# Performance work log

Measured on AMD Instinct MI355X. Metric: run time of the kernel, lower is better.

Reference implementation:

```python
import jax, jax.numpy as jnp
import numpy as np

H, W, C = 96, 96, 21
THETA_ALPHA, THETA_BETA, THETA_GAMMA = 8.0, 0.125, 3.0
NUM_ITERATIONS = 5


def setup_inputs() -> dict:
    key = jax.random.key(0)
    k1, k2, k3, k4, k5 = jax.random.split(key, 5)
    unaries = jax.random.normal(k1, (1, H, W, C), dtype=jnp.float32)
    reference_image = jax.random.uniform(k2, (1, H, W, 3), dtype=jnp.float32)
    # truncated normal(mean=0, std=0.1) as in tf.initializers.truncated_normal
    spatial_ker_weights = 0.1 * jax.random.truncated_normal(k3, -2.0, 2.0, (C,), dtype=jnp.float32)
    bilateral_ker_weights = 0.1 * jax.random.truncated_normal(k4, -2.0, 2.0, (C,), dtype=jnp.float32)
    compatibility_matrix = 0.1 * jax.random.truncated_normal(k5, -2.0, 2.0, (C, C), dtype=jnp.float32)
    return {
        "unaries": unaries,
        "reference_image": reference_image,
        "spatial_ker_weights": spatial_ker_weights,
        "bilateral_ker_weights": bilateral_ker_weights,
        "compatibility_matrix": compatibility_matrix,
    }


def _gaussian_kernel(feats):
    # feats: [B, N, D] -> K[b, i, j] = exp(-0.5 * ||f_i - f_j||^2)
    sq = jnp.sum(feats * feats, axis=-1)  # [B, N]
    d2 = sq[:, :, None] + sq[:, None, :] - 2.0 * jnp.einsum("bnd,bmd->bnm", feats, feats)
    return jnp.exp(-0.5 * jnp.maximum(d2, 0.0))


def _build_kernels(reference_image):
    # Exact-math equivalent of the permutohedral lattice Gaussian filter:
    # spatial features = positions/theta_gamma; bilateral = [pos/theta_alpha, rgb/theta_beta].
    B = reference_image.shape[0]
    yy, xx = jnp.meshgrid(jnp.arange(H, dtype=jnp.float32), jnp.arange(W, dtype=jnp.float32), indexing="ij")
    pos = jnp.stack([yy, xx], axis=-1).reshape(1, H * W, 2)  # [1, N, 2]
    pos = jnp.broadcast_to(pos, (B, H * W, 2))
    col = reference_image.reshape(B, H * W, 3)
    k_spatial = _gaussian_kernel(pos / THETA_GAMMA)
    k_bilateral = _gaussian_kernel(jnp.concatenate([pos / THETA_ALPHA, col / THETA_BETA], axis=-1))
    return k_spatial, k_bilateral


def reference(unaries, reference_image, spatial_ker_weights, bilateral_ker_weights, compatibility_matrix):
    B = unaries.shape[0]
    N = H * W
    k_spatial, k_bilateral = _build_kernels(reference_image)  # built once; reused each iteration
    u = unaries.reshape(B, N, C)
    q = u
    for _ in range(NUM_ITERATIONS):
        q = jax.nn.softmax(q, axis=-1)
        spatial_out = jnp.einsum("bnm,bmc->bnc", k_spatial, q)
        bilateral_out = jnp.einsum("bnm,bmc->bnc", k_bilateral, q)
        # pairwise^T = compat @ diag(w_s) @ S^T + compat @ diag(w_b) @ Bi^T
        # => pairwise = (S * w_s + Bi * w_b) @ compat^T
        message = spatial_out * spatial_ker_weights + bilateral_out * bilateral_ker_weights
        pairwise = message @ compatibility_matrix.T
        q = u - pairwise
    return q.reshape(unaries.shape)
```

## Files before the change

kernel.cpp:

```cpp
#include <hip/hip_runtime.h>
#include <hip/hip_bf16.h>
#include <algorithm>
#include <cmath>

#define HH 96
#define WW 96
#define CC 21
#define NN (HH*WW)
#define NELEM (NN*CC)
#define RS 20
#define NPAR (2*CC + CC*CC)
#define L2E 1.4426950408889634f
#define MSTEPS 24
#define NBB (36*24)
#define NSTRIP 8
#define NBLUR (CC*NSTRIP)
#define SROWS 12
#define TRUNC2 1225
#define BLURKEY 0x10000

typedef short bf16x8 __attribute__((ext_vector_type(8)));
typedef float f32x16 __attribute__((ext_vector_type(16)));

__device__ __forceinline__ float fexp2(float x) { return __builtin_amdgcn_exp2f(x); }
__device__ __forceinline__ float fexp(float x)  { return __builtin_amdgcn_exp2f(x * L2E); }

__device__ __forceinline__ short f2b(float f) {
    __hip_bfloat16 h = __float2bfloat16(f);
    short s; __builtin_memcpy(&s, &h, 2); return s;
}

__global__ void k_sniff(const unsigned short* __restrict__ u16, int* __restrict__ flag32) {
    __shared__ int sfound;
    if (threadIdx.x == 0) sfound = 0;
    __syncthreads();
    const int base = blockIdx.x * (NELEM/32);
    int found = 0;
    for (int i = base + threadIdx.x; i < base + NELEM/32; i += 256) {
        unsigned v = u16[i];
        if ((v & 0x7F80u) == 0x7F80u) found = 1;
    }
    if (found) sfound = 1;
    __syncthreads();
    if (threadIdx.x == 0) flag32[blockIdx.x] = sfound;
}

__device__ __forceinline__ int rdflag(const int* __restrict__ flag32) {
    int f = 0;
    #pragma unroll
    for (int i = 0; i < 32; i++) f |= flag32[i];
    return f;
}

__global__ __launch_bounds__(256) void k_prep(
    const void* __restrict__ u, const void* __restrict__ img,
    const void* __restrict__ wS, const void* __restrict__ wB,
    const void* __restrict__ compat, const int* __restrict__ flag32,
    float* __restrict__ uf, float* __restrict__ featx, float* __restrict__ par,
    float* __restrict__ bil, __hip_bfloat16* __restrict__ pT)
{
    const int f = rdflag(flag32);
    const int tid = threadIdx.x;
    const int n = blockIdx.x * 256 + tid;

    if (blockIdx.x == 0) {
        for (int i = tid; i < NPAR; i += 256) {
            const void* src; int j;
            if (i < CC)        { src = wS;     j = i; }
            else if (i < 2*CC) { src = wB;     j = i - CC; }
            else               { src = compat; j = i - 2*CC; }
            par[i] = f ? ((const float*)src)[j]
                       : __bfloat162float(((const __hip_bfloat16*)src)[j]);
        }
    }

    {
        float c0, c1, c2;
        if (f) { const float* p = (const float*)img;
                 c0 = p[3*n]; c1 = p[3*n+1]; c2 = p[3*n+2]; }
        else   { const __hip_bfloat16* p = (const __hip_bfloat16*)img;
                 c0 = __bfloat162float(p[3*n]); c1 = __bfloat162float(p[3*n+1]);
                 c2 = __bfloat162float(p[3*n+2]); }
        float ym = (float)(n / WW), xm = (float)(n % WW);
        const float sc = 0.15014029f;
        const float cf = 9.6089787f;
        featx[8*n + 0] = -L2E * (fmaf(ym, ym, xm*xm) * 0.0078125f
                                 + 32.f * (c0*c0 + c1*c1 + c2*c2));
        featx[8*n + 1] = sc * ym;
        featx[8*n + 2] = sc * xm;
        featx[8*n + 3] = cf * c0;
        featx[8*n + 4] = cf * c1;
        featx[8*n + 5] = cf * c2;
        featx[8*n + 6] = 0.f;
        featx[8*n + 7] = 0.f;
    }

    float v[CC];
    float mx = -1e30f;
    #pragma unroll
    for (int c = 0; c < CC; c++) {
        float uv = f ? ((const float*)u)[n*CC + c]
                     : __bfloat162float(((const __hip_bfloat16*)u)[n*CC + c]);
        uf[n*CC + c] = uv;
        v[c] = uv;
        mx = fmaxf(mx, uv);
    }
    float s = 0.f;
    #pragma unroll
    for (int c = 0; c < CC; c++) { v[c] = fexp(v[c] - mx); s += v[c]; }
    float inv = 1.f / s;
    #pragma unroll
    for (int c = 0; c < CC; c++) {
        pT[(size_t)c*NN + n] = __float2bfloat16(v[c] * inv);
        bil[(size_t)c*NN + n] = 0.f;
    }
}

__global__ __launch_bounds__(256) void k_work(
    const __hip_bfloat16* __restrict__ pT,
    const float* __restrict__ featx,
    float* __restrict__ bil,
    float* __restrict__ s2T,
    const int* __restrict__ tab)
{
    __shared__ float smem[6176];
    const int tid = threadIdx.x;
    const int item = tab[blockIdx.x];

    if (item < BLURKEY) {
        float* lds_h = smem;
        const int wv   = tid >> 6, lane = tid & 63;
        const int quad = lane >> 5, lid = lane & 31;

        const int nt = item >> 5, mc = item & 31;
        const int ny0 = (nt / 6) * 16, nx0 = (nt % 6) * 16;
        const int my0 = (mc & 3) * 24, mx0 = (mc >> 2) * 16;

        const int dx = (mx0 > nx0 + 15) ? mx0 - (nx0 + 15)
                     : ((nx0 > mx0 + 15) ? nx0 - (mx0 + 15) : 0);
        const int lim = TRUNC2 - dx * dx;
        int T = (int)sqrtf((float)lim);
        T -= (T * T > lim);
        T += ((T + 1) * (T + 1) <= lim);

        int blo = ny0 - T - my0;      blo = blo < 0 ? 0 : blo;
        int bhi = ny0 + 15 + T - my0; bhi = bhi > 23 ? 23 : bhi;

        {
            float4* dst = (float4*)lds_h;
            for (int i = blo * 32 + tid; i < (bhi + 1) * 32; i += 256) {
                const int seg = i >> 5, off = i & 31;
                dst[i] = ((const float4*)(featx +
                          (size_t)((my0 + seg) * WW + mx0) * 8))[off];
            }
        }
        __syncthreads();

        const int by0 = ny0 + 4 * wv;
        int lo = by0 - T - my0;     lo = lo < 0 ? 0 : lo;
        int hi = by0 + 3 + T - my0; hi = hi > 23 ? 23 : hi;
        if (lo > hi) return;

        const int row = lid >> 4, col = lid & 15;
        const int n0 = (by0 + row) * WW + nx0 + col;
        const int n1 = n0 + 2 * WW;
        const float4 g0a = *(const float4*)(featx + (size_t)n0 * 8);
        const float4 g0b = *(const float4*)(featx + (size_t)n0 * 8 + 4);
        const float4 g1a = *(const float4*)(featx + (size_t)n1 * 8);
        const float4 g1b = *(const float4*)(featx + (size_t)n1 * 8 + 4);

        f32x16 acc0, acc1;
        #pragma unroll
        for (int r = 0; r < 16; r++) { acc0[r] = 0.f; acc1[r] = 0.f; }

        int mg = (my0 + lo) * WW + mx0 + quad * 8;
        #pragma unroll 1
        for (int step = lo; step <= hi; step++, mg += WW) {
            bf16x8 afrag = *(const bf16x8*)(pT + (size_t)lid * NN + mg);

            const float* h = lds_h + (step * 16 + quad * 8) * 8;
            float kb0[8], kb1[8];
            #pragma unroll
            for (int j = 0; j < 8; j++) {
                float4 ha = *(const float4*)(h + j * 8);
                float4 hb = *(const float4*)(h + j * 8 + 4);
                float s0 = g0a.x + ha.x;
                s0 = fmaf(g0a.y, ha.y, s0);
                s0 = fmaf(g0a.z, ha.z, s0);
                s0 = fmaf(g0a.w, ha.w, s0);
                s0 = fmaf(g0b.x, hb.x, s0);
                s0 = fmaf(g0b.y, hb.y, s0);
                kb0[j] = fexp2(s0);
                float s1 = g1a.x + ha.x;
                s1 = fmaf(g1a.y, ha.y, s1);
                s1 = fmaf(g1a.z, ha.z, s1);
                s1 = fmaf(g1a.w, ha.w, s1);
                s1 = fmaf(g1b.x, hb.x, s1);
                s1 = fmaf(g1b.y, hb.y, s1);
                kb1[j] = fexp2(s1);
            }
            bf16x8 b0, b1;
            #pragma unroll
            for (int j = 0; j < 8; j++) { b0[j] = f2b(kb0[j]); b1[j] = f2b(kb1[j]); }

            acc0 = __builtin_amdgcn_mfma_f32_32x32x16_bf16(afrag, b0, acc0, 0, 0, 0);
            acc1 = __builtin_amdgcn_mfma_f32_32x32x16_bf16(afrag, b1, acc1, 0, 0, 0);
        }

        #pragma unroll
        for (int r = 0; r < 16; r++) {
            int c = (r & 3) + 8 * (r >> 2) + 4 * quad;
            if (c < CC) {
                atomicAdd(&bil[(size_t)c * NN + n0], acc0[r]);
                atomicAdd(&bil[(size_t)c * NN + n1], acc1[r]);
            }
        }
    } else {
        __shared__ float w_s[RS + 1];
        float* A  = smem;
        float* B2 = smem + 4992;

        const int b2 = item - BLURKEY;
        const int c = b2 % CC;
        const int strip = b2 / CC;
        const int y0 = strip * SROWS;
        const int ylo = (y0 - RS < 0) ? 0 : y0 - RS;
        const int yhi = (y0 + SROWS - 1 + RS > HH - 1) ? HH - 1 : y0 + SROWS - 1 + RS;
        const int nrows = yhi - ylo + 1;

        if (tid <= RS) w_s[tid] = fexp2(-(float)(tid*tid) * (L2E / 18.f));
        const __hip_bfloat16* src = pT + (size_t)c * NN + ylo * WW;
        for (int i = tid; i < nrows * WW; i += 256)
            A[i] = __bfloat162float(src[i]);
        __syncthreads();

        for (int i = tid; i < SROWS * WW; i += 256) {
            const int yo = y0 + i / WW;
            const int x  = i % WW;
            float acc = A[(yo - ylo) * WW + x];
            #pragma unroll
            for (int d = 1; d <= RS; d++) {
                float s = 0.f;
                if (yo - d >= 0)  s += A[(yo - d - ylo) * WW + x];
                if (yo + d < HH)  s += A[(yo + d - ylo) * WW + x];
                acc = fmaf(w_s[d], s, acc);
            }
            B2[i] = acc;
        }
        __syncthreads();

        for (int i = tid; i < SROWS * WW; i += 256) {
            const int r = i / WW, x = i % WW;
            float acc = B2[i];
            #pragma unroll
            for (int d = 1; d <= RS; d++) {
                float s = 0.f;
                if (x - d >= 0)  s += B2[r * WW + x - d];
                if (x + d < WW)  s += B2[r * WW + x + d];
                acc = fmaf(w_s[d], s, acc);
            }
            s2T[(size_t)c * NN + (y0 + r) * WW + x] = acc;
        }
    }
}

__global__ __launch_bounds__(256) void k_update(
    float* __restrict__ bil, const float* __restrict__ s2T,
    const float* __restrict__ uf, const float* __restrict__ par,
    const int* __restrict__ flag32,
    __hip_bfloat16* __restrict__ pT, void* __restrict__ out, int last)
{
    __shared__ float sc[CC*CC + 1];
    __shared__ float sws[CC], swb[CC];
    const int tid = threadIdx.x;
    for (int i = tid; i < CC*CC; i += 256) sc[i] = par[2*CC + i];
    if (tid == 0) sc[CC*CC] = 0.f;
    if (tid < CC) { sws[tid] = par[tid]; swb[tid] = par[CC + tid]; }
    __syncthreads();

    const int half = tid & 1;
    const int n = blockIdx.x * 128 + (tid >> 1);

    float msg[11];
    #pragma unroll
    for (int k = 0; k < 11; k++) {
        const int cp = 2*k + half;
        if (cp < CC) {
            msg[k] = fmaf(s2T[(size_t)cp*NN + n], sws[cp],
                          bil[(size_t)cp*NN + n] * swb[cp]);
            bil[(size_t)cp*NN + n] = 0.f;
        } else msg[k] = 0.f;
    }

    float pw[CC];
    #pragma unroll
    for (int c = 0; c < CC; c++) {
        float a = msg[0] * sc[c*CC + half];
        #pragma unroll
        for (int k = 1; k < 11; k++)
            a = fmaf(msg[k], sc[c*CC + 2*k + half], a);
        pw[c] = a;
    }
    #pragma unroll
    for (int c = 0; c < CC; c++)
        pw[c] += __shfl_xor(pw[c], 1, 64);

    float qv[CC];
    float mx = -1e30f;
    #pragma unroll
    for (int c = 0; c < CC; c++) {
        qv[c] = uf[(size_t)n*CC + c] - pw[c];
        mx = fmaxf(mx, qv[c]);
    }

    if (last) {
        const int is_f32 = rdflag(flag32);
        #pragma unroll
        for (int k = 0; k < 11; k++) {
            const int ce = 2*k, co = (k < 10) ? 2*k + 1 : 0;
            float v = half ? qv[co] : qv[ce];
            const int c = 2*k + half;
            if (c < CC) {
                if (is_f32) ((float*)out)[(size_t)n*CC + c] = v;
                else ((__hip_bfloat16*)out)[(size_t)n*CC + c] = __float2bfloat16(v);
            }
        }
    } else {
        float ex[11]; float ssum = 0.f;
        #pragma unroll
        for (int k = 0; k < 11; k++) {
            const int ce = 2*k, co = (k < 10) ? 2*k + 1 : 0;
            float v = half ? qv[co] : qv[ce];
            float e = fexp(v - mx);
            if (2*k + half < CC) ssum += e;
            ex[k] = e;
        }
        ssum += __shfl_xor(ssum, 1, 64);
        const float inv = 1.f / ssum;
        #pragma unroll
        for (int k = 0; k < 11; k++) {
            const int c = 2*k + half;
            if (c < CC) pT[(size_t)c*NN + n] = __float2bfloat16(ex[k] * inv);
        }
    }
}

extern "C" void kernel_launch(void* const* d_in, const int* in_sizes, int n_in,
                              void* d_out, int out_size, void* d_ws, size_t ws_size,
                              hipStream_t stream)
{
    static int h_tab[NBB + NBLUR];
    static int h_n = 0;
    if (h_n == 0) {
        struct It { int key; int cost; };
        static It its[NBB + NBLUR];
        int m = 0;
        for (int nt = 0; nt < 36; nt++)
            for (int mc = 0; mc < 24; mc++) {
                const int ny0 = (nt / 6) * 16, nx0 = (nt % 6) * 16;
                const int my0 = (mc & 3) * 24, mx0 = (mc >> 2) * 16;
                const int dx = (mx0 > nx0 + 15) ? mx0 - (nx0 + 15)
                             : ((nx0 > mx0 + 15) ? nx0 - (mx0 + 15) : 0);
                const int lim = TRUNC2 - dx * dx;
                if (lim < 0) continue;
                int T = (int)std::sqrt((double)lim);
                while (T * T > lim) T--;
                while ((T + 1) * (T + 1) <= lim) T++;
                int cost = 0;
                for (int wv = 0; wv < 4; wv++) {
                    const int by0 = ny0 + 4 * wv;
                    int lo = by0 - T - my0;     if (lo < 0)  lo = 0;
                    int hi = by0 + 3 + T - my0; if (hi > 23) hi = 23;
                    if (lo <= hi) cost += hi - lo + 1;
                }
                if (cost == 0) continue;
                its[m].key = (nt << 5) | mc; its[m].cost = cost; m++;
            }
        for (int b = 0; b < NBLUR; b++) { its[m].key = BLURKEY + b; its[m].cost = 20; m++; }
        std::sort(its, its + m, [](const It& a, const It& b) { return a.cost > b.cost; });
        for (int i = 0; i < m; i++) h_tab[i] = its[i].key;
        h_n = m;
    }

    float* ws = (float*)d_ws;
    int*   flag32 = (int*)ws;
    float* par    = ws + 32;
    float* featx  = ws + 544;
    __hip_bfloat16* pT = (__hip_bfloat16*)(ws + 74272);
    float* uf  = ws + 74272 + 147456;
    float* s2T = uf + NELEM;
    float* bil = s2T + NELEM;
    int*   d_tab = (int*)(bil + NELEM);

    hipMemcpyAsync(d_tab, h_tab, h_n * sizeof(int), hipMemcpyHostToDevice, stream);

    k_sniff<<<32, 256, 0, stream>>>((const unsigned short*)d_in[0], flag32);
    k_prep<<<NN/256, 256, 0, stream>>>(d_in[0], d_in[1], d_in[2], d_in[3], d_in[4],
                                       flag32, uf, featx, par, bil, pT);

    for (int it = 0; it < 5; it++) {
        k_work<<<h_n, 256, 0, stream>>>(pT, featx, bil, s2T, d_tab);
        k_update<<<NN/128, 256, 0, stream>>>(bil, s2T, uf, par, flag32,
                                             pT, d_out, (it == 4) ? 1 : 0);
    }
}
```

Measured before the change: 237.9 us.

## Bin bilateral m-chunks per tile into register-accumulated slots instead of atomics

Work items for the bilateral product are regrouped on the host so that each output tile gets up to eight load-balanced bins of m-chunks. Each block loops over its chunks, accumulating in MFMA registers, then writes plain stores to a per-slot buffer instead of issuing float atomicAdds. The update kernel sums the eight slots and zeroes them. This removes atomic contention and per-block setup overhead. In exchange, each iteration reads and clears eight full-size slot buffers, and each block does more serial work and sync per chunk.

```diff
diff --git a/kernel.cpp b/kernel.cpp
--- a/kernel.cpp
+++ b/kernel.cpp
@@ -1,6 +1,7 @@
 #include <hip/hip_runtime.h>
 #include <hip/hip_bf16.h>
 #include <algorithm>
+#include <vector>
 #include <cmath>
 
 #define HH 96
@@ -11,13 +12,11 @@
 #define RS 20
 #define NPAR (2*CC + CC*CC)
 #define L2E 1.4426950408889634f
-#define MSTEPS 24
-#define NBB (36*24)
-#define NSTRIP 8
-#define NBLUR (CC*NSTRIP)
+#define NSLOT 8
 #define SROWS 12
+#define NBLUR (CC*8)
 #define TRUNC2 1225
-#define BLURKEY 0x10000
+#define BLURFLAG 0x40000000
 
 typedef short bf16x8 __attribute__((ext_vector_type(8)));
 typedef float f32x16 __attribute__((ext_vector_type(16)));
@@ -57,7 +56,7 @@
     const void* __restrict__ wS, const void* __restrict__ wB,
     const void* __restrict__ compat, const int* __restrict__ flag32,
     float* __restrict__ uf, float* __restrict__ featx, float* __restrict__ par,
-    float* __restrict__ bil, __hip_bfloat16* __restrict__ pT)
+    float* __restrict__ bil8, __hip_bfloat16* __restrict__ pT)
 {
     const int f = rdflag(flag32);
     const int tid = threadIdx.x;
@@ -73,7 +72,6 @@
                        : __bfloat162float(((const __hip_bfloat16*)src)[j]);
         }
     }
-
     {
         float c0, c1, c2;
         if (f) { const float* p = (const float*)img;
@@ -112,56 +110,80 @@
     #pragma unroll
     for (int c = 0; c < CC; c++) {
         pT[(size_t)c*NN + n] = __float2bfloat16(v[c] * inv);
-        bil[(size_t)c*NN + n] = 0.f;
+        #pragma unroll
+        for (int sl = 0; sl < NSLOT; sl++)
+            bil8[((size_t)sl*CC + c)*NN + n] = 0.f;
+    }
+}
+
+__device__ __forceinline__ void blur_item(
+    int b2, float* smem, const __hip_bfloat16* __restrict__ pT,
+    float* __restrict__ s2T, int tid)
+{
+    float* A   = smem;
+    float* B2  = smem + 4992;
+    float* w_s = smem + 6144;
+    const int c = b2 % CC;
+    const int strip = b2 / CC;
+    const int y0 = strip * SROWS;
+    const int ylo = (y0 - RS < 0) ? 0 : y0 - RS;
+    const int yhi = (y0 + SROWS - 1 + RS > HH - 1) ? HH - 1 : y0 + SROWS - 1 + RS;
+    const int nrows = yhi - ylo + 1;
+
+    if (tid <= RS) w_s[tid] = fexp2(-(float)(tid*tid) * (L2E / 18.f));
+    const __hip_bfloat16* src = pT + (size_t)c * NN + ylo * WW;
+    for (int i = tid; i < nrows * WW; i += 256)
+        A[i] = __bfloat162float(src[i]);
+    __syncthreads();
+
+    for (int i = tid; i < SROWS * WW; i += 256) {
+        const int yo = y0 + i / WW;
+        const int x  = i % WW;
+        float acc = A[(yo - ylo) * WW + x];
+        #pragma unroll
+        for (int d = 1; d <= RS; d++) {
+            float s = 0.f;
+            if (yo - d >= 0)  s += A[(yo - d - ylo) * WW + x];
+            if (yo + d < HH)  s += A[(yo + d - ylo) * WW + x];
+            acc = fmaf(w_s[d], s, acc);
+        }
+        B2[i] = acc;
+    }
+    __syncthreads();
+
+    for (int i = tid; i < SROWS * WW; i += 256) {
+        const int r = i / WW, x = i % WW;
+        float acc = B2[i];
+        #pragma unroll
+        for (int d = 1; d <= RS; d++) {
+            float s = 0.f;
+            if (x - d >= 0)  s += B2[r * WW + x - d];
+            if (x + d < WW)  s += B2[r * WW + x + d];
+            acc = fmaf(w_s[d], s, acc);
+        }
+        s2T[(size_t)c * NN + (y0 + r) * WW + x] = acc;
     }
 }
 
 __global__ __launch_bounds__(256) void k_work(
-    const __hip_bfloat16* __restrict__ pT,
-    const float* __restrict__ featx,
-    float* __restrict__ bil,
-    float* __restrict__ s2T,
-    const int* __restrict__ tab)
+    const __hip_bfloat16* __restrict__ pT, const float* __restrict__ featx,
+    float* __restrict__ bil8, float* __restrict__ s2T,
+    const int* __restrict__ hdr, const int* __restrict__ mcs)
 {
     __shared__ float smem[6176];
     const int tid = threadIdx.x;
-    const int item = tab[blockIdx.x];
-
-    if (item < BLURKEY) {
-        float* lds_h = smem;
-        const int wv   = tid >> 6, lane = tid & 63;
+    const int item = hdr[blockIdx.x];
+
+    if (!(item & BLURFLAG)) {
+        const int nt   = item >> 18;
+        const int slot = (item >> 15) & 7;
+        const int off  = (item >> 5) & 1023;
+        const int cnt  = item & 31;
+        const int ny0 = (nt / 6) * 16, nx0 = (nt % 6) * 16;
+        const int wv = tid >> 6, lane = tid & 63;
         const int quad = lane >> 5, lid = lane & 31;
-
-        const int nt = item >> 5, mc = item & 31;
-        const int ny0 = (nt / 6) * 16, nx0 = (nt % 6) * 16;
-        const int my0 = (mc & 3) * 24, mx0 = (mc >> 2) * 16;
-
-        const int dx = (mx0 > nx0 + 15) ? mx0 - (nx0 + 15)
-                     : ((nx0 > mx0 + 15) ? nx0 - (mx0 + 15) : 0);
-        const int lim = TRUNC2 - dx * dx;
-        int T = (int)sqrtf((float)lim);
-        T -= (T * T > lim);
-        T += ((T + 1) * (T + 1) <= lim);
-
-        int blo = ny0 - T - my0;      blo = blo < 0 ? 0 : blo;
-        int bhi = ny0 + 15 + T - my0; bhi = bhi > 23 ? 23 : bhi;
-
-        {
-            float4* dst = (float4*)lds_h;
-            for (int i = blo * 32 + tid; i < (bhi + 1) * 32; i += 256) {
-                const int seg = i >> 5, off = i & 31;
-                dst[i] = ((const float4*)(featx +
-                          (size_t)((my0 + seg) * WW + mx0) * 8))[off];
-            }
-        }
-        __syncthreads();
-
+        const int row = lid >> 4, col = lid & 15;
         const int by0 = ny0 + 4 * wv;
-        int lo = by0 - T - my0;     lo = lo < 0 ? 0 : lo;
-        int hi = by0 + 3 + T - my0; hi = hi > 23 ? 23 : hi;
-        if (lo > hi) return;
-
-        const int row = lid >> 4, col = lid & 15;
         const int n0 = (by0 + row) * WW + nx0 + col;
         const int n1 = n0 + 2 * WW;
         const float4 g0a = *(const float4*)(featx + (size_t)n0 * 8);
@@ -173,99 +195,77 @@
         #pragma unroll
         for (int r = 0; r < 16; r++) { acc0[r] = 0.f; acc1[r] = 0.f; }
 
-        int mg = (my0 + lo) * WW + mx0 + quad * 8;
-        #pragma unroll 1
-        for (int step = lo; step <= hi; step++, mg += WW) {
-            bf16x8 afrag = *(const bf16x8*)(pT + (size_t)lid * NN + mg);
-
-            const float* h = lds_h + (step * 16 + quad * 8) * 8;
-            float kb0[8], kb1[8];
-            #pragma unroll
-            for (int j = 0; j < 8; j++) {
-                float4 ha = *(const float4*)(h + j * 8);
-                float4 hb = *(const float4*)(h + j * 8 + 4);
-                float s0 = g0a.x + ha.x;
-                s0 = fmaf(g0a.y, ha.y, s0);
-                s0 = fmaf(g0a.z, ha.z, s0);
-                s0 = fmaf(g0a.w, ha.w, s0);
-                s0 = fmaf(g0b.x, hb.x, s0);
-                s0 = fmaf(g0b.y, hb.y, s0);
-                kb0[j] = fexp2(s0);
-                float s1 = g1a.x + ha.x;
-                s1 = fmaf(g1a.y, ha.y, s1);
-                s1 = fmaf(g1a.z, ha.z, s1);
-                s1 = fmaf(g1a.w, ha.w, s1);
-                s1 = fmaf(g1b.x, hb.x, s1);
-                s1 = fmaf(g1b.y, hb.y, s1);
-                kb1[j] = fexp2(s1);
-            }
-            bf16x8 b0, b1;
-            #pragma unroll
-            for (int j = 0; j < 8; j++) { b0[j] = f2b(kb0[j]); b1[j] = f2b(kb1[j]); }
-
-            acc0 = __builtin_amdgcn_mfma_f32_32x32x16_bf16(afrag, b0, acc0, 0, 0, 0);
-            acc1 = __builtin_amdgcn_mfma_f32_32x32x16_bf16(afrag, b1, acc1, 0, 0, 0);
+        for (int ci = 0; ci < cnt; ci++) {
+            const int mc = mcs[off + ci];
+            const int my0 = (mc & 3) * 24, mx0 = (mc >> 2) * 16;
+            const int dx = (mx0 > nx0 + 15) ? mx0 - (nx0 + 15)
+                         : ((nx0 > mx0 + 15) ? nx0 - (mx0 + 15) : 0);
+            const int lim = TRUNC2 - dx * dx;
+            int T = (int)sqrtf((float)lim);
+            T -= (T * T > lim);
+            T += ((T + 1) * (T + 1) <= lim);
+            int blo = ny0 - T - my0;      blo = blo < 0 ? 0 : blo;
+            int bhi = ny0 + 15 + T - my0; bhi = bhi > 23 ? 23 : bhi;
+
+            __syncthreads();
+            {
+                float4* dst = (float4*)smem;
+                for (int i = blo * 32 + tid; i < (bhi + 1) * 32; i += 256) {
+                    const int seg = i >> 5, o = i & 31;
+                    dst[i] = ((const float4*)(featx +
+                              (size_t)((my0 + seg) * WW + mx0) * 8))[o];
+                }
+            }
+            __syncthreads();
+
+            int lo = by0 - T - my0;     lo = lo < 0 ? 0 : lo;
+            int hi = by0 + 3 + T - my0; hi = hi > 23 ? 23 : hi;
+            if (lo <= hi) {
+                int mg = (my0 + lo) * WW + mx0 + quad * 8;
+                #pragma unroll 1
+                for (int step = lo; step <= hi; step++, mg += WW) {
+                    bf16x8 afrag = *(const bf16x8*)(pT + (size_t)lid * NN + mg);
+                    const float* h = smem + (step * 16 + quad * 8) * 8;
+                    float kb0[8], kb1[8];
+                    #pragma unroll
+                    for (int j = 0; j < 8; j++) {
+                        float4 ha = *(const float4*)(h + j * 8);
+                        float4 hb = *(const float4*)(h + j * 8 + 4);
+                        float s0 = g0a.x + ha.x;
+                        s0 = fmaf(g0a.y, ha.y, s0); s0 = fmaf(g0a.z, ha.z, s0);
+                        s0 = fmaf(g0a.w, ha.w, s0); s0 = fmaf(g0b.x, hb.x, s0);
+                        s0 = fmaf(g0b.y, hb.y, s0);
+                        kb0[j] = fexp2(s0);
+                        float s1 = g1a.x + ha.x;
+                        s1 = fmaf(g1a.y, ha.y, s1); s1 = fmaf(g1a.z, ha.z, s1);
+                        s1 = fmaf(g1a.w, ha.w, s1); s1 = fmaf(g1b.x, hb.x, s1);
+                        s1 = fmaf(g1b.y, hb.y, s1);
+                        kb1[j] = fexp2(s1);
+                    }
+                    bf16x8 b0, b1;
+                    #pragma unroll
+                    for (int j = 0; j < 8; j++) { b0[j] = f2b(kb0[j]); b1[j] = f2b(kb1[j]); }
+                    acc0 = __builtin_amdgcn_mfma_f32_32x32x16_bf16(afrag, b0, acc0, 0, 0, 0);
+                    acc1 = __builtin_amdgcn_mfma_f32_32x32x16_bf16(afrag, b1, acc1, 0, 0, 0);
+                }
+            }
         }
 
         #pragma unroll
         for (int r = 0; r < 16; r++) {
             int c = (r & 3) + 8 * (r >> 2) + 4 * quad;
             if (c < CC) {
-                atomicAdd(&bil[(size_t)c * NN + n0], acc0[r]);
-                atomicAdd(&bil[(size_t)c * NN + n1], acc1[r]);
+                bil8[((size_t)slot*CC + c)*NN + n0] = acc0[r];
+                bil8[((size_t)slot*CC + c)*NN + n1] = acc1[r];
             }
         }
     } else {
-        __shared__ float w_s[RS + 1];
-        float* A  = smem;
-        float* B2 = smem + 4992;
-
-        const int b2 = item - BLURKEY;
-        const int c = b2 % CC;
-        const int strip = b2 / CC;
-        const int y0 = strip * SROWS;
-        const int ylo = (y0 - RS < 0) ? 0 : y0 - RS;
-        const int yhi = (y0 + SROWS - 1 + RS > HH - 1) ? HH - 1 : y0 + SROWS - 1 + RS;
-        const int nrows = yhi - ylo + 1;
-
-        if (tid <= RS) w_s[tid] = fexp2(-(float)(tid*tid) * (L2E / 18.f));
-        const __hip_bfloat16* src = pT + (size_t)c * NN + ylo * WW;
-        for (int i = tid; i < nrows * WW; i += 256)
-            A[i] = __bfloat162float(src[i]);
-        __syncthreads();
-
-        for (int i = tid; i < SROWS * WW; i += 256) {
-            const int yo = y0 + i / WW;
-            const int x  = i % WW;
-            float acc = A[(yo - ylo) * WW + x];
-            #pragma unroll
-            for (int d = 1; d <= RS; d++) {
-                float s = 0.f;
-                if (yo - d >= 0)  s += A[(yo - d - ylo) * WW + x];
-                if (yo + d < HH)  s += A[(yo + d - ylo) * WW + x];
-                acc = fmaf(w_s[d], s, acc);
-            }
-            B2[i] = acc;
-        }
-        __syncthreads();
-
-        for (int i = tid; i < SROWS * WW; i += 256) {
-            const int r = i / WW, x = i % WW;
-            float acc = B2[i];
-            #pragma unroll
-            for (int d = 1; d <= RS; d++) {
-                float s = 0.f;
-                if (x - d >= 0)  s += B2[r * WW + x - d];
-                if (x + d < WW)  s += B2[r * WW + x + d];
-                acc = fmaf(w_s[d], s, acc);
-            }
-            s2T[(size_t)c * NN + (y0 + r) * WW + x] = acc;
-        }
+        blur_item(item & 0xFFFF, smem, pT, s2T, tid);
     }
 }
 
 __global__ __launch_bounds__(256) void k_update(
-    float* __restrict__ bil, const float* __restrict__ s2T,
+    float* __restrict__ bil8, const float* __restrict__ s2T,
     const float* __restrict__ uf, const float* __restrict__ par,
     const int* __restrict__ flag32,
     __hip_bfloat16* __restrict__ pT, void* __restrict__ out, int last)
@@ -286,9 +286,14 @@
     for (int k = 0; k < 11; k++) {
         const int cp = 2*k + half;
         if (cp < CC) {
-            msg[k] = fmaf(s2T[(size_t)cp*NN + n], sws[cp],
-                          bil[(size_t)cp*NN + n] * swb[cp]);
-            bil[(size_t)cp*NN + n] = 0.f;
+            float b = 0.f;
+            #pragma unroll
+            for (int sl = 0; sl < NSLOT; sl++)
+                b += bil8[((size_t)sl*CC + cp)*NN + n];
+            msg[k] = fmaf(s2T[(size_t)cp*NN + n], sws[cp], b * swb[cp]);
+            #pragma unroll
+            for (int sl = 0; sl < NSLOT; sl++)
+                bil8[((size_t)sl*CC + cp)*NN + n] = 0.f;
         } else msg[k] = 0.f;
     }
 
@@ -349,37 +354,64 @@
                               void* d_out, int out_size, void* d_ws, size_t ws_size,
                               hipStream_t stream)
 {
-    static int h_tab[NBB + NBLUR];
-    static int h_n = 0;
-    if (h_n == 0) {
-        struct It { int key; int cost; };
-        static It its[NBB + NBLUR];
-        int m = 0;
-        for (int nt = 0; nt < 36; nt++)
+    static std::vector<int> h_buf;
+    static int h_nb = 0;
+    if (h_nb == 0) {
+        struct Rec { int blur, b2, nt, slot; long load; std::vector<int> mc; };
+        std::vector<Rec> recs;
+        for (int nt = 0; nt < 36; nt++) {
+            const int ny0 = (nt/6)*16, nx0 = (nt%6)*16;
+            struct It { int mc; int cost; };
+            std::vector<It> v; long tot = 0;
             for (int mc = 0; mc < 24; mc++) {
-                const int ny0 = (nt / 6) * 16, nx0 = (nt % 6) * 16;
-                const int my0 = (mc & 3) * 24, mx0 = (mc >> 2) * 16;
-                const int dx = (mx0 > nx0 + 15) ? mx0 - (nx0 + 15)
-                             : ((nx0 > mx0 + 15) ? nx0 - (mx0 + 15) : 0);
-                const int lim = TRUNC2 - dx * dx;
+                const int my0 = (mc&3)*24, mx0 = (mc>>2)*16;
+                const int dx = (mx0 > nx0+15) ? mx0-(nx0+15)
+                             : ((nx0 > mx0+15) ? nx0-(mx0+15) : 0);
+                const int lim = TRUNC2 - dx*dx;
                 if (lim < 0) continue;
                 int T = (int)std::sqrt((double)lim);
-                while (T * T > lim) T--;
-                while ((T + 1) * (T + 1) <= lim) T++;
+                while (T*T > lim) T--;
+                while ((T+1)*(T+1) <= lim) T++;
                 int cost = 0;
                 for (int wv = 0; wv < 4; wv++) {
-                    const int by0 = ny0 + 4 * wv;
+                    const int by0 = ny0 + 4*wv;
                     int lo = by0 - T - my0;     if (lo < 0)  lo = 0;
                     int hi = by0 + 3 + T - my0; if (hi > 23) hi = 23;
                     if (lo <= hi) cost += hi - lo + 1;
                 }
                 if (cost == 0) continue;
-                its[m].key = (nt << 5) | mc; its[m].cost = cost; m++;
-            }
-        for (int b = 0; b < NBLUR; b++) { its[m].key = BLURKEY + b; its[m].cost = 20; m++; }
-        std::sort(its, its + m, [](const It& a, const It& b) { return a.cost > b.cost; });
-        for (int i = 0; i < m; i++) h_tab[i] = its[i].key;
-        h_n = m;
+                v.push_back({mc, cost}); tot += cost;
+            }
+            if (v.empty()) continue;
+            int nb = (int)std::min<long>(NSLOT, (tot + 159) / 160);
+            if (nb > (int)v.size()) nb = (int)v.size();
+            std::sort(v.begin(), v.end(),
+                      [](const It& a, const It& b){ return a.cost > b.cost; });
+            std::vector<Rec> bins(nb);
+            for (int i = 0; i < nb; i++) { bins[i] = {0, 0, nt, i, 0, {}}; }
+            for (auto& it : v) {
+                int bmin = 0;
+                for (int i = 1; i < nb; i++)
+                    if (bins[i].load < bins[bmin].load) bmin = i;
+                bins[bmin].load += it.cost;
+                bins[bmin].mc.push_back(it.mc);
+            }
+            for (auto& b : bins) recs.push_back(std::move(b));
+        }
+        for (int b = 0; b < NBLUR; b++) recs.push_back({1, b, 0, 0, 20, {}});
+        std::sort(recs.begin(), recs.end(),
+                  [](const Rec& a, const Rec& b){ return a.load > b.load; });
+        const int nb = (int)recs.size();
+        h_buf.assign(nb, 0);
+        int off = 0;
+        for (int i = 0; i < nb; i++) {
+            if (recs[i].blur) { h_buf[i] = BLURFLAG | recs[i].b2; continue; }
+            const int cnt = (int)recs[i].mc.size();
+            h_buf[i] = (recs[i].nt << 18) | (recs[i].slot << 15) | (off << 5) | cnt;
+            for (int m : recs[i].mc) h_buf.push_back(m);
+            off += cnt;
+        }
+        h_nb = nb;
     }
 
     float* ws = (float*)d_ws;
@@ -387,20 +419,24 @@
     float* par    = ws + 32;
     float* featx  = ws + 544;
     __hip_bfloat16* pT = (__hip_bfloat16*)(ws + 74272);
-    float* uf  = ws + 74272 + 147456;
-    float* s2T = uf + NELEM;
-    float* bil = s2T + NELEM;
-    int*   d_tab = (int*)(bil + NELEM);
-
-    hipMemcpyAsync(d_tab, h_tab, h_n * sizeof(int), hipMemcpyHostToDevice, stream);
+    float* uf   = ws + 221728;
+    float* s2T  = uf + NELEM;
+    float* bil8 = s2T + NELEM;
+    int*   d_tab = (int*)(bil8 + (size_t)NSLOT*NELEM);
+
+    hipMemcpyAsync(d_tab, h_buf.data(), h_buf.size() * sizeof(int),
+                   hipMemcpyHostToDevice, stream);
+
+    const int* d_hdr = d_tab;
+    const int* d_mcs = d_tab + h_nb;
 
     k_sniff<<<32, 256, 0, stream>>>((const unsigned short*)d_in[0], flag32);
     k_prep<<<NN/256, 256, 0, stream>>>(d_in[0], d_in[1], d_in[2], d_in[3], d_in[4],
-                                       flag32, uf, featx, par, bil, pT);
+                                       flag32, uf, featx, par, bil8, pT);
 
     for (int it = 0; it < 5; it++) {
-        k_work<<<h_n, 256, 0, stream>>>(pT, featx, bil, s2T, d_tab);
-        k_update<<<NN/128, 256, 0, stream>>>(bil, s2T, uf, par, flag32,
+        k_work<<<h_nb, 256, 0, stream>>>(pT, featx, bil8, s2T, d_hdr, d_mcs);
+        k_update<<<NN/128, 256, 0, stream>>>(bil8, s2T, uf, par, flag32,
                                              pT, d_out, (it == 4) ? 1 : 0);
     }
 }
```

Result: slower. 284.5 us (+19.6%).

## Replace bilateral atomics with per-slot partial buffers reduced in update kernel

Applied to the files above, without the earlier changes.

Each bilateral work block now writes its partial sums to a dedicated slot buffer, with up to 24 slots per output tile, using plain stores instead of float atomicAdd. The update kernel sums over the active slots for each pixel tile, which also removes the zeroing of the accumulator in prep and update. The aim is to avoid atomic contention and read-modify-write traffic. The cost is a much larger workspace and more reads in k_update. Minor extras: feature loads shrink from float4 to float2, and k_update is relaunched with 128-thread blocks.

```diff
diff --git a/kernel.cpp b/kernel.cpp
--- a/kernel.cpp
+++ b/kernel.cpp
@@ -1,6 +1,7 @@
 #include <hip/hip_runtime.h>
 #include <hip/hip_bf16.h>
 #include <algorithm>
+#include <vector>
 #include <cmath>
 
 #define HH 96
@@ -11,13 +12,11 @@
 #define RS 20
 #define NPAR (2*CC + CC*CC)
 #define L2E 1.4426950408889634f
-#define MSTEPS 24
-#define NBB (36*24)
-#define NSTRIP 8
-#define NBLUR (CC*NSTRIP)
+#define NBLUR (CC*8)
 #define SROWS 12
 #define TRUNC2 1225
 #define BLURKEY 0x10000
+#define NSLOT 24
 
 typedef short bf16x8 __attribute__((ext_vector_type(8)));
 typedef float f32x16 __attribute__((ext_vector_type(16)));
@@ -57,7 +56,7 @@
     const void* __restrict__ wS, const void* __restrict__ wB,
     const void* __restrict__ compat, const int* __restrict__ flag32,
     float* __restrict__ uf, float* __restrict__ featx, float* __restrict__ par,
-    float* __restrict__ bil, __hip_bfloat16* __restrict__ pT)
+    __hip_bfloat16* __restrict__ pT)
 {
     const int f = rdflag(flag32);
     const int tid = threadIdx.x;
@@ -73,7 +72,6 @@
                        : __bfloat162float(((const __hip_bfloat16*)src)[j]);
         }
     }
-
     {
         float c0, c1, c2;
         if (f) { const float* p = (const float*)img;
@@ -110,22 +108,21 @@
     for (int c = 0; c < CC; c++) { v[c] = fexp(v[c] - mx); s += v[c]; }
     float inv = 1.f / s;
     #pragma unroll
-    for (int c = 0; c < CC; c++) {
+    for (int c = 0; c < CC; c++)
         pT[(size_t)c*NN + n] = __float2bfloat16(v[c] * inv);
-        bil[(size_t)c*NN + n] = 0.f;
-    }
 }
 
 __global__ __launch_bounds__(256) void k_work(
     const __hip_bfloat16* __restrict__ pT,
     const float* __restrict__ featx,
-    float* __restrict__ bil,
+    float* __restrict__ bil24,
     float* __restrict__ s2T,
     const int* __restrict__ tab)
 {
     __shared__ float smem[6176];
     const int tid = threadIdx.x;
-    const int item = tab[blockIdx.x];
+    const int item = tab[2*blockIdx.x];
+    const int slot = tab[2*blockIdx.x + 1];
 
     if (item < BLURKEY) {
         float* lds_h = smem;
@@ -159,67 +156,68 @@
         const int by0 = ny0 + 4 * wv;
         int lo = by0 - T - my0;     lo = lo < 0 ? 0 : lo;
         int hi = by0 + 3 + T - my0; hi = hi > 23 ? 23 : hi;
-        if (lo > hi) return;
 
         const int row = lid >> 4, col = lid & 15;
         const int n0 = (by0 + row) * WW + nx0 + col;
         const int n1 = n0 + 2 * WW;
         const float4 g0a = *(const float4*)(featx + (size_t)n0 * 8);
-        const float4 g0b = *(const float4*)(featx + (size_t)n0 * 8 + 4);
+        const float2 g0b = *(const float2*)(featx + (size_t)n0 * 8 + 4);
         const float4 g1a = *(const float4*)(featx + (size_t)n1 * 8);
-        const float4 g1b = *(const float4*)(featx + (size_t)n1 * 8 + 4);
+        const float2 g1b = *(const float2*)(featx + (size_t)n1 * 8 + 4);
 
         f32x16 acc0, acc1;
         #pragma unroll
         for (int r = 0; r < 16; r++) { acc0[r] = 0.f; acc1[r] = 0.f; }
 
-        int mg = (my0 + lo) * WW + mx0 + quad * 8;
-        #pragma unroll 1
-        for (int step = lo; step <= hi; step++, mg += WW) {
-            bf16x8 afrag = *(const bf16x8*)(pT + (size_t)lid * NN + mg);
-
-            const float* h = lds_h + (step * 16 + quad * 8) * 8;
-            float kb0[8], kb1[8];
-            #pragma unroll
-            for (int j = 0; j < 8; j++) {
-                float4 ha = *(const float4*)(h + j * 8);
-                float4 hb = *(const float4*)(h + j * 8 + 4);
-                float s0 = g0a.x + ha.x;
-                s0 = fmaf(g0a.y, ha.y, s0);
-                s0 = fmaf(g0a.z, ha.z, s0);
-                s0 = fmaf(g0a.w, ha.w, s0);
-                s0 = fmaf(g0b.x, hb.x, s0);
-                s0 = fmaf(g0b.y, hb.y, s0);
-                kb0[j] = fexp2(s0);
-                float s1 = g1a.x + ha.x;
-                s1 = fmaf(g1a.y, ha.y, s1);
-                s1 = fmaf(g1a.z, ha.z, s1);
-                s1 = fmaf(g1a.w, ha.w, s1);
-                s1 = fmaf(g1b.x, hb.x, s1);
-                s1 = fmaf(g1b.y, hb.y, s1);
-                kb1[j] = fexp2(s1);
-            }
-            bf16x8 b0, b1;
-            #pragma unroll
-            for (int j = 0; j < 8; j++) { b0[j] = f2b(kb0[j]); b1[j] = f2b(kb1[j]); }
-
-            acc0 = __builtin_amdgcn_mfma_f32_32x32x16_bf16(afrag, b0, acc0, 0, 0, 0);
-            acc1 = __builtin_amdgcn_mfma_f32_32x32x16_bf16(afrag, b1, acc1, 0, 0, 0);
-        }
-
+        if (lo <= hi) {
+            int mg = (my0 + lo) * WW + mx0 + quad * 8;
+            #pragma unroll 1
+            for (int step = lo; step <= hi; step++, mg += WW) {
+                bf16x8 afrag = *(const bf16x8*)(pT + (size_t)lid * NN + mg);
+
+                const float* h = lds_h + (step * 16 + quad * 8) * 8;
+                float kb0[8], kb1[8];
+                #pragma unroll
+                for (int j = 0; j < 8; j++) {
+                    float4 ha = *(const float4*)(h + j * 8);
+                    float2 hb = *(const float2*)(h + j * 8 + 4);
+                    float s0 = g0a.x + ha.x;
+                    s0 = fmaf(g0a.y, ha.y, s0);
+                    s0 = fmaf(g0a.z, ha.z, s0);
+                    s0 = fmaf(g0a.w, ha.w, s0);
+                    s0 = fmaf(g0b.x, hb.x, s0);
+                    s0 = fmaf(g0b.y, hb.y, s0);
+                    kb0[j] = fexp2(s0);
+                    float s1 = g1a.x + ha.x;
+                    s1 = fmaf(g1a.y, ha.y, s1);
+                    s1 = fmaf(g1a.z, ha.z, s1);
+                    s1 = fmaf(g1a.w, ha.w, s1);
+                    s1 = fmaf(g1b.x, hb.x, s1);
+                    s1 = fmaf(g1b.y, hb.y, s1);
+                    kb1[j] = fexp2(s1);
+                }
+                bf16x8 b0, b1;
+                #pragma unroll
+                for (int j = 0; j < 8; j++) { b0[j] = f2b(kb0[j]); b1[j] = f2b(kb1[j]); }
+
+                acc0 = __builtin_amdgcn_mfma_f32_32x32x16_bf16(afrag, b0, acc0, 0, 0, 0);
+                acc1 = __builtin_amdgcn_mfma_f32_32x32x16_bf16(afrag, b1, acc1, 0, 0, 0);
+            }
+        }
+
+        float* dst = bil24 + (size_t)slot * CC * NN;
         #pragma unroll
         for (int r = 0; r < 16; r++) {
             int c = (r & 3) + 8 * (r >> 2) + 4 * quad;
             if (c < CC) {
-                atomicAdd(&bil[(size_t)c * NN + n0], acc0[r]);
-                atomicAdd(&bil[(size_t)c * NN + n1], acc1[r]);
+                dst[(size_t)c * NN + n0] = acc0[r];
+                dst[(size_t)c * NN + n1] = acc1[r];
             }
         }
     } else {
-        __shared__ float w_s[RS + 1];
-        float* A  = smem;
-        float* B2 = smem + 4992;
-
+        float* A   = smem;
+        float* B2  = smem + 4992;
+        float* w_s = smem + 6144;
         const int b2 = item - BLURKEY;
         const int c = b2 % CC;
         const int strip = b2 / CC;
@@ -264,32 +262,45 @@
     }
 }
 
-__global__ __launch_bounds__(256) void k_update(
-    float* __restrict__ bil, const float* __restrict__ s2T,
+__global__ __launch_bounds__(128) void k_update(
+    const float* __restrict__ bil24, const float* __restrict__ s2T,
     const float* __restrict__ uf, const float* __restrict__ par,
-    const int* __restrict__ flag32,
+    const int* __restrict__ flag32, const int* __restrict__ cnt_tab,
     __hip_bfloat16* __restrict__ pT, void* __restrict__ out, int last)
 {
     __shared__ float sc[CC*CC + 1];
     __shared__ float sws[CC], swb[CC];
     const int tid = threadIdx.x;
-    for (int i = tid; i < CC*CC; i += 256) sc[i] = par[2*CC + i];
+    for (int i = tid; i < CC*CC; i += 128) sc[i] = par[2*CC + i];
     if (tid == 0) sc[CC*CC] = 0.f;
     if (tid < CC) { sws[tid] = par[tid]; swb[tid] = par[CC + tid]; }
     __syncthreads();
 
     const int half = tid & 1;
-    const int n = blockIdx.x * 128 + (tid >> 1);
+    const int n = blockIdx.x * 64 + (tid >> 1);
+    const int nt = ((n / WW) >> 4) * 6 + ((n % WW) >> 4);
+    const int cnt = cnt_tab[nt];
+
+    float mb[11];
+    #pragma unroll
+    for (int k = 0; k < 11; k++) mb[k] = 0.f;
+    #pragma unroll 1
+    for (int sl = 0; sl < cnt; sl++) {
+        const float* base = bil24 + (size_t)sl * CC * NN + n;
+        #pragma unroll
+        for (int k = 0; k < 11; k++) {
+            const int cp = 2*k + half;
+            if (cp < CC) mb[k] += base[(size_t)cp * NN];
+        }
+    }
 
     float msg[11];
     #pragma unroll
     for (int k = 0; k < 11; k++) {
         const int cp = 2*k + half;
-        if (cp < CC) {
-            msg[k] = fmaf(s2T[(size_t)cp*NN + n], sws[cp],
-                          bil[(size_t)cp*NN + n] * swb[cp]);
-            bil[(size_t)cp*NN + n] = 0.f;
-        } else msg[k] = 0.f;
+        if (cp < CC)
+            msg[k] = fmaf(s2T[(size_t)cp*NN + n], sws[cp], mb[k] * swb[cp]);
+        else msg[k] = 0.f;
     }
 
     float pw[CC];
@@ -349,37 +360,45 @@
                               void* d_out, int out_size, void* d_ws, size_t ws_size,
                               hipStream_t stream)
 {
-    static int h_tab[NBB + NBLUR];
+    static std::vector<int> h_tab;
+    static int h_cnt[36];
     static int h_n = 0;
     if (h_n == 0) {
-        struct It { int key; int cost; };
-        static It its[NBB + NBLUR];
-        int m = 0;
-        for (int nt = 0; nt < 36; nt++)
+        struct It { int key, slot, cost; };
+        std::vector<It> its;
+        for (int nt = 0; nt < 36; nt++) {
+            h_cnt[nt] = 0;
+            const int ny0 = (nt/6)*16, nx0 = (nt%6)*16;
             for (int mc = 0; mc < 24; mc++) {
-                const int ny0 = (nt / 6) * 16, nx0 = (nt % 6) * 16;
-                const int my0 = (mc & 3) * 24, mx0 = (mc >> 2) * 16;
-                const int dx = (mx0 > nx0 + 15) ? mx0 - (nx0 + 15)
-                             : ((nx0 > mx0 + 15) ? nx0 - (mx0 + 15) : 0);
-                const int lim = TRUNC2 - dx * dx;
+                const int my0 = (mc&3)*24, mx0 = (mc>>2)*16;
+                const int dx = (mx0 > nx0+15) ? mx0-(nx0+15)
+                             : ((nx0 > mx0+15) ? nx0-(mx0+15) : 0);
+                const int lim = TRUNC2 - dx*dx;
                 if (lim < 0) continue;
                 int T = (int)std::sqrt((double)lim);
-                while (T * T > lim) T--;
-                while ((T + 1) * (T + 1) <= lim) T++;
+                while (T*T > lim) T--;
+                while ((T+1)*(T+1) <= lim) T++;
                 int cost = 0;
                 for (int wv = 0; wv < 4; wv++) {
-                    const int by0 = ny0 + 4 * wv;
+                    const int by0 = ny0 + 4*wv;
                     int lo = by0 - T - my0;     if (lo < 0)  lo = 0;
                     int hi = by0 + 3 + T - my0; if (hi > 23) hi = 23;
                     if (lo <= hi) cost += hi - lo + 1;
                 }
                 if (cost == 0) continue;
-                its[m].key = (nt << 5) | mc; its[m].cost = cost; m++;
-            }
-        for (int b = 0; b < NBLUR; b++) { its[m].key = BLURKEY + b; its[m].cost = 20; m++; }
-        std::sort(its, its + m, [](const It& a, const It& b) { return a.cost > b.cost; });
-        for (int i = 0; i < m; i++) h_tab[i] = its[i].key;
-        h_n = m;
+                its.push_back({(nt << 5) | mc, h_cnt[nt]++, cost});
+            }
+        }
+        for (int b = 0; b < NBLUR; b++) its.push_back({BLURKEY + b, 0, 20});
+        std::sort(its.begin(), its.end(),
+                  [](const It& a, const It& b) { return a.cost > b.cost; });
+        h_n = (int)its.size();
+        h_tab.resize(2 * h_n + 36);
+        for (int i = 0; i < h_n; i++) {
+            h_tab[2*i]     = its[i].key;
+            h_tab[2*i + 1] = its[i].slot;
+        }
+        for (int t = 0; t < 36; t++) h_tab[2*h_n + t] = h_cnt[t];
     }
 
     float* ws = (float*)d_ws;
@@ -387,20 +406,22 @@
     float* par    = ws + 32;
     float* featx  = ws + 544;
     __hip_bfloat16* pT = (__hip_bfloat16*)(ws + 74272);
-    float* uf  = ws + 74272 + 147456;
-    float* s2T = uf + NELEM;
-    float* bil = s2T + NELEM;
-    int*   d_tab = (int*)(bil + NELEM);
-
-    hipMemcpyAsync(d_tab, h_tab, h_n * sizeof(int), hipMemcpyHostToDevice, stream);
+    float* uf    = ws + 221728;
+    float* s2T   = uf + NELEM;
+    float* bil24 = s2T + NELEM;
+    int*   d_tab = (int*)(bil24 + (size_t)NSLOT*NELEM);
+    const int* d_cnt = d_tab + 2*h_n;
+
+    hipMemcpyAsync(d_tab, h_tab.data(), h_tab.size() * sizeof(int),
+                   hipMemcpyHostToDevice, stream);
 
     k_sniff<<<32, 256, 0, stream>>>((const unsigned short*)d_in[0], flag32);
     k_prep<<<NN/256, 256, 0, stream>>>(d_in[0], d_in[1], d_in[2], d_in[3], d_in[4],
-                                       flag32, uf, featx, par, bil, pT);
+                                       flag32, uf, featx, par, pT);
 
     for (int it = 0; it < 5; it++) {
-        k_work<<<h_n, 256, 0, stream>>>(pT, featx, bil, s2T, d_tab);
-        k_update<<<NN/128, 256, 0, stream>>>(bil, s2T, uf, par, flag32,
-                                             pT, d_out, (it == 4) ? 1 : 0);
-    }
-}
+        k_work<<<h_n, 256, 0, stream>>>(pT, featx, bil24, s2T, d_tab);
+        k_update<<<NN/64, 128, 0, stream>>>(bil24, s2T, uf, par, flag32, d_cnt,
+                                            pT, d_out, (it == 4) ? 1 : 0);
+    }
+}
```

Measured after the change: 365.7 us. +53.8%, slower.

## Add pixel-major bf16 probability copy and compile-time work table

Applied to the files above, without the earlier changes.

Adds a second copy of the softmax probabilities in pixel-major layout (32 padded channels per pixel), written by the prep and update kernels. The MFMA A-fragment in the kernel-matrix pass now reads from this copy with strided 16-bit loads instead of 8 contiguous bf16 from the channel-major array. The work-item table is now built at compile time into constant memory, which removes the per-call host-to-device copy. The cost is an extra scattered write of the probabilities each iteration, and the A-fragment is now assembled from eight separate short loads.

```diff
diff --git a/kernel.cpp b/kernel.cpp
--- a/kernel.cpp
+++ b/kernel.cpp
@@ -1,7 +1,5 @@
 #include <hip/hip_runtime.h>
 #include <hip/hip_bf16.h>
-#include <algorithm>
-#include <cmath>
 
 #define HH 96
 #define WW 96
@@ -11,10 +9,8 @@
 #define RS 20
 #define NPAR (2*CC + CC*CC)
 #define L2E 1.4426950408889634f
-#define MSTEPS 24
 #define NBB (36*24)
-#define NSTRIP 8
-#define NBLUR (CC*NSTRIP)
+#define NBLUR (CC*8)
 #define SROWS 12
 #define TRUNC2 1225
 #define BLURKEY 0x10000
@@ -25,10 +21,45 @@
 __device__ __forceinline__ float fexp2(float x) { return __builtin_amdgcn_exp2f(x); }
 __device__ __forceinline__ float fexp(float x)  { return __builtin_amdgcn_exp2f(x * L2E); }
 
-__device__ __forceinline__ short f2b(float f) {
+__device__ __forceinline__ unsigned short f2u(float f) {
     __hip_bfloat16 h = __float2bfloat16(f);
-    short s; __builtin_memcpy(&s, &h, 2); return s;
-}
+    unsigned short s; __builtin_memcpy(&s, &h, 2); return s;
+}
+
+struct Tab { int n; int k[NBB + NBLUR]; };
+constexpr Tab build_tab() {
+    Tab t{};
+    int key[NBB + NBLUR] = {};
+    int cst[NBB + NBLUR] = {};
+    int m = 0;
+    for (int nt = 0; nt < 36; nt++)
+        for (int mc = 0; mc < 24; mc++) {
+            const int ny0 = (nt / 6) * 16, nx0 = (nt % 6) * 16;
+            const int my0 = (mc & 3) * 24, mx0 = (mc >> 2) * 16;
+            const int dx = (mx0 > nx0 + 15) ? mx0 - (nx0 + 15)
+                         : ((nx0 > mx0 + 15) ? nx0 - (mx0 + 15) : 0);
+            const int lim = TRUNC2 - dx * dx;
+            if (lim < 0) continue;
+            int T = 0;
+            while ((T + 1) * (T + 1) <= lim) T++;
+            int cost = 0;
+            for (int wv = 0; wv < 4; wv++) {
+                const int by0 = ny0 + 4 * wv;
+                int lo = by0 - T - my0;     if (lo < 0)  lo = 0;
+                int hi = by0 + 3 + T - my0; if (hi > 23) hi = 23;
+                if (lo <= hi) cost += hi - lo + 1;
+            }
+            if (cost == 0) continue;
+            key[m] = (nt << 5) | mc; cst[m] = cost; m++;
+        }
+    for (int b = 0; b < NBLUR; b++) { key[m] = BLURKEY + b; cst[m] = 20; m++; }
+    for (int c = 96; c >= 1; c--)
+        for (int i = 0; i < m; i++)
+            if (cst[i] == c) t.k[t.n++] = key[i];
+    return t;
+}
+constexpr Tab TT = build_tab();
+__device__ __constant__ Tab c_TT = TT;
 
 __global__ void k_sniff(const unsigned short* __restrict__ u16, int* __restrict__ flag32) {
     __shared__ int sfound;
@@ -57,7 +88,8 @@
     const void* __restrict__ wS, const void* __restrict__ wB,
     const void* __restrict__ compat, const int* __restrict__ flag32,
     float* __restrict__ uf, float* __restrict__ featx, float* __restrict__ par,
-    float* __restrict__ bil, __hip_bfloat16* __restrict__ pT)
+    float* __restrict__ bil, __hip_bfloat16* __restrict__ pT,
+    unsigned short* __restrict__ pT2)
 {
     const int f = rdflag(flag32);
     const int tid = threadIdx.x;
@@ -73,7 +105,6 @@
                        : __bfloat162float(((const __hip_bfloat16*)src)[j]);
         }
     }
-
     {
         float c0, c1, c2;
         if (f) { const float* p = (const float*)img;
@@ -109,23 +140,39 @@
     #pragma unroll
     for (int c = 0; c < CC; c++) { v[c] = fexp(v[c] - mx); s += v[c]; }
     float inv = 1.f / s;
+
+    unsigned short ub[CC];
     #pragma unroll
     for (int c = 0; c < CC; c++) {
-        pT[(size_t)c*NN + n] = __float2bfloat16(v[c] * inv);
+        float pv = v[c] * inv;
+        ub[c] = f2u(pv);
+        __hip_bfloat16 h; __builtin_memcpy(&h, &ub[c], 2);
+        pT[(size_t)c*NN + n] = h;
         bil[(size_t)c*NN + n] = 0.f;
     }
+    unsigned dw[16];
+    #pragma unroll
+    for (int d = 0; d < 16; d++) {
+        unsigned lo = (2*d     < CC) ? (unsigned)ub[2*d]     : 0u;
+        unsigned hi = (2*d + 1 < CC) ? (unsigned)ub[2*d + 1] : 0u;
+        dw[d] = lo | (hi << 16);
+    }
+    unsigned* q = (unsigned*)(pT2 + (size_t)n * 32);
+    #pragma unroll
+    for (int d = 0; d < 4; d++)
+        *(uint4*)(q + 4*d) = *(uint4*)&dw[4*d];
 }
 
 __global__ __launch_bounds__(256) void k_work(
     const __hip_bfloat16* __restrict__ pT,
+    const unsigned short* __restrict__ pT2,
     const float* __restrict__ featx,
     float* __restrict__ bil,
-    float* __restrict__ s2T,
-    const int* __restrict__ tab)
+    float* __restrict__ s2T)
 {
     __shared__ float smem[6176];
     const int tid = threadIdx.x;
-    const int item = tab[blockIdx.x];
+    const int item = c_TT.k[blockIdx.x];
 
     if (item < BLURKEY) {
         float* lds_h = smem;
@@ -173,10 +220,13 @@
         #pragma unroll
         for (int r = 0; r < 16; r++) { acc0[r] = 0.f; acc1[r] = 0.f; }
 
-        int mg = (my0 + lo) * WW + mx0 + quad * 8;
+        const int mg0 = (my0 + lo) * WW + mx0 + quad * 8;
+        const unsigned short* ap = pT2 + (size_t)mg0 * 32 + lid;
         #pragma unroll 1
-        for (int step = lo; step <= hi; step++, mg += WW) {
-            bf16x8 afrag = *(const bf16x8*)(pT + (size_t)lid * NN + mg);
+        for (int step = lo; step <= hi; step++, ap += WW * 32) {
+            bf16x8 afrag;
+            #pragma unroll
+            for (int j = 0; j < 8; j++) afrag[j] = (short)ap[j * 32];
 
             const float* h = lds_h + (step * 16 + quad * 8) * 8;
             float kb0[8], kb1[8];
@@ -201,7 +251,10 @@
             }
             bf16x8 b0, b1;
             #pragma unroll
-            for (int j = 0; j < 8; j++) { b0[j] = f2b(kb0[j]); b1[j] = f2b(kb1[j]); }
+            for (int j = 0; j < 8; j++) {
+                b0[j] = (short)f2u(kb0[j]);
+                b1[j] = (short)f2u(kb1[j]);
+            }
 
             acc0 = __builtin_amdgcn_mfma_f32_32x32x16_bf16(afrag, b0, acc0, 0, 0, 0);
             acc1 = __builtin_amdgcn_mfma_f32_32x32x16_bf16(afrag, b1, acc1, 0, 0, 0);
@@ -216,10 +269,9 @@
             }
         }
     } else {
-        __shared__ float w_s[RS + 1];
-        float* A  = smem;
-        float* B2 = smem + 4992;
-
+        float* A   = smem;
+        float* B2  = smem + 4992;
+        float* w_s = smem + 6144;
         const int b2 = item - BLURKEY;
         const int c = b2 % CC;
         const int strip = b2 / CC;
@@ -268,7 +320,8 @@
     float* __restrict__ bil, const float* __restrict__ s2T,
     const float* __restrict__ uf, const float* __restrict__ par,
     const int* __restrict__ flag32,
-    __hip_bfloat16* __restrict__ pT, void* __restrict__ out, int last)
+    __hip_bfloat16* __restrict__ pT, unsigned short* __restrict__ pT2,
+    void* __restrict__ out, int last)
 {
     __shared__ float sc[CC*CC + 1];
     __shared__ float sws[CC], swb[CC];
@@ -337,10 +390,34 @@
         }
         ssum += __shfl_xor(ssum, 1, 64);
         const float inv = 1.f / ssum;
+
+        unsigned short b[11];
         #pragma unroll
         for (int k = 0; k < 11; k++) {
             const int c = 2*k + half;
-            if (c < CC) pT[(size_t)c*NN + n] = __float2bfloat16(ex[k] * inv);
+            if (c < CC) {
+                float pv = ex[k] * inv;
+                b[k] = f2u(pv);
+                __hip_bfloat16 h; __builtin_memcpy(&h, &b[k], 2);
+                pT[(size_t)c*NN + n] = h;
+            } else b[k] = 0;
+        }
+        unsigned dw[16];
+        #pragma unroll
+        for (int d = 0; d < 16; d++) {
+            unsigned mine  = (d < 11) ? (unsigned)b[d] : 0u;
+            unsigned other = (unsigned)__shfl_xor((int)mine, 1, 64) & 0xFFFFu;
+            unsigned lo = half ? other : mine;
+            unsigned hi = half ? mine  : other;
+            dw[d] = lo | (hi << 16);
+        }
+        unsigned* q = (unsigned*)(pT2 + (size_t)n * 32);
+        if (half == 0) {
+            *(uint4*)(q + 0) = *(uint4*)&dw[0];
+            *(uint4*)(q + 4) = *(uint4*)&dw[4];
+        } else {
+            *(uint4*)(q + 8)  = *(uint4*)&dw[8];
+            *(uint4*)(q + 12) = *(uint4*)&dw[12];
         }
     }
 }
@@ -349,58 +426,23 @@
                               void* d_out, int out_size, void* d_ws, size_t ws_size,
                               hipStream_t stream)
 {
-    static int h_tab[NBB + NBLUR];
-    static int h_n = 0;
-    if (h_n == 0) {
-        struct It { int key; int cost; };
-        static It its[NBB + NBLUR];
-        int m = 0;
-        for (int nt = 0; nt < 36; nt++)
-            for (int mc = 0; mc < 24; mc++) {
-                const int ny0 = (nt / 6) * 16, nx0 = (nt % 6) * 16;
-                const int my0 = (mc & 3) * 24, mx0 = (mc >> 2) * 16;
-                const int dx = (mx0 > nx0 + 15) ? mx0 - (nx0 + 15)
-                             : ((nx0 > mx0 + 15) ? nx0 - (mx0 + 15) : 0);
-                const int lim = TRUNC2 - dx * dx;
-                if (lim < 0) continue;
-                int T = (int)std::sqrt((double)lim);
-                while (T * T > lim) T--;
-                while ((T + 1) * (T + 1) <= lim) T++;
-                int cost = 0;
-                for (int wv = 0; wv < 4; wv++) {
-                    const int by0 = ny0 + 4 * wv;
-                    int lo = by0 - T - my0;     if (lo < 0)  lo = 0;
-                    int hi = by0 + 3 + T - my0; if (hi > 23) hi = 23;
-                    if (lo <= hi) cost += hi - lo + 1;
-                }
-                if (cost == 0) continue;
-                its[m].key = (nt << 5) | mc; its[m].cost = cost; m++;
-            }
-        for (int b = 0; b < NBLUR; b++) { its[m].key = BLURKEY + b; its[m].cost = 20; m++; }
-        std::sort(its, its + m, [](const It& a, const It& b) { return a.cost > b.cost; });
-        for (int i = 0; i < m; i++) h_tab[i] = its[i].key;
-        h_n = m;
-    }
-
     float* ws = (float*)d_ws;
     int*   flag32 = (int*)ws;
     float* par    = ws + 32;
     float* featx  = ws + 544;
     __hip_bfloat16* pT = (__hip_bfloat16*)(ws + 74272);
-    float* uf  = ws + 74272 + 147456;
+    unsigned short* pT2 = (unsigned short*)(ws + 221728);
+    float* uf  = ws + 369184;
     float* s2T = uf + NELEM;
     float* bil = s2T + NELEM;
-    int*   d_tab = (int*)(bil + NELEM);
-
-    hipMemcpyAsync(d_tab, h_tab, h_n * sizeof(int), hipMemcpyHostToDevice, stream);
 
     k_sniff<<<32, 256, 0, stream>>>((const unsigned short*)d_in[0], flag32);
     k_prep<<<NN/256, 256, 0, stream>>>(d_in[0], d_in[1], d_in[2], d_in[3], d_in[4],
-                                       flag32, uf, featx, par, bil, pT);
+                                       flag32, uf, featx, par, bil, pT, pT2);
 
     for (int it = 0; it < 5; it++) {
-        k_work<<<h_n, 256, 0, stream>>>(pT, featx, bil, s2T, d_tab);
+        k_work<<<TT.n, 256, 0, stream>>>(pT, pT2, featx, bil, s2T);
         k_update<<<NN/128, 256, 0, stream>>>(bil, s2T, uf, par, flag32,
-                                             pT, d_out, (it == 4) ? 1 : 0);
-    }
-}
+                                             pT, pT2, d_out, (it == 4) ? 1 : 0);
+    }
+}
```

New measurement: 246.9 us. 3.8% more time.
